# Optimization experiments

Hardware: AMD Instinct MI355X
Metric: run time of the kernel (lower is better)

The kernel has to match this reference:

```python
import jax, jax.numpy as jnp
import numpy as np

VOCAB, EMB, HID, LAYERS = 32000, 512, 512, 2
B, S = 16, 256


def setup_inputs() -> dict:
    key = jax.random.key(0)
    ks = jax.random.split(key, 8)
    x = jax.random.randint(ks[0], (B, S), 0, VOCAB)
    emb = jax.random.normal(ks[1], (VOCAB, EMB), dtype=jnp.float32) * 0.02
    # input_dim == hidden_dim == 512, so per-layer weights can be stacked
    Wih = jax.random.normal(ks[2], (LAYERS, 4 * HID, EMB), dtype=jnp.float32) * 0.05
    Whh = jax.random.normal(ks[3], (LAYERS, 4 * HID, HID), dtype=jnp.float32) * 0.05
    b = jax.random.normal(ks[4], (LAYERS, 4 * HID), dtype=jnp.float32) * 0.05
    fc_w = jax.random.normal(ks[5], (VOCAB, HID), dtype=jnp.float32) * 0.02
    fc_b = jnp.zeros((VOCAB,), dtype=jnp.float32)
    return {"x": x, "emb": emb, "Wih": Wih, "Whh": Whh, "b": b, "fc_w": fc_w, "fc_b": fc_b}


def reference(x, emb, Wih, Whh, b, fc_w, fc_b):
    L = Wih.shape[0]
    Bsz = x.shape[0]
    H = Whh.shape[-1]
    xe = emb[x]  # (B, S, E)
    h0 = jnp.zeros((L, Bsz, H), dtype=emb.dtype)
    c0 = jnp.zeros((L, Bsz, H), dtype=emb.dtype)

    def step(carry, xt):  # xt: (B, E)
        h, c = carry
        inp = xt
        hs, cs = [], []
        for l in range(L):  # small fixed layer loop
            gates = inp @ Wih[l].T + h[l] @ Whh[l].T + b[l]  # (B, 4H)
            i, f, g, o = jnp.split(gates, 4, axis=1)
            cn = jax.nn.sigmoid(f) * c[l] + jax.nn.sigmoid(i) * jnp.tanh(g)
            hn = jax.nn.sigmoid(o) * jnp.tanh(cn)
            hs.append(hn)
            cs.append(cn)
            inp = hn
        return (jnp.stack(hs), jnp.stack(cs)), inp

    _, outs = jax.lax.scan(step, (h0, c0), jnp.swapaxes(xe, 0, 1))  # outs: (S, B, H)
    outs = jnp.swapaxes(outs, 0, 1)  # (B, S, H); dropout is identity (eval)
    logits = outs @ fc_w.T + fc_b  # (B, S, V)
    return logits
```

## Files before the change

### kernel.cpp

```cpp
#include <hip/hip_runtime.h>
#include <hip/hip_bf16.h>

#define SEQ 256
#define NB 16
#define HID 512
#define VOC 32000

typedef short bf16x8 __attribute__((ext_vector_type(8)));
typedef float f32x4 __attribute__((ext_vector_type(4)));
typedef unsigned long long u64;

__device__ __forceinline__ void ld_lds16(const void* g, void* l) {
  __builtin_amdgcn_global_load_lds((const __attribute__((address_space(1))) void*)g,
                                   (__attribute__((address_space(3))) void*)l, 16, 0, 0);
}

__device__ __forceinline__ float sigf(float x) { return 1.0f / (1.0f + expf(-x)); }

__device__ __forceinline__ unsigned pk2(float a, float b) {
  __hip_bfloat16 ha = __float2bfloat16(a), hb = __float2bfloat16(b);
  unsigned short ua = *(unsigned short*)&ha, ub = *(unsigned short*)&hb;
  return (unsigned)ua | ((unsigned)ub << 16);
}

__device__ __forceinline__ u64 agload(const u64* p) {
  return __hip_atomic_load(p, __ATOMIC_RELAXED, __HIP_MEMORY_SCOPE_AGENT);
}
__device__ __forceinline__ void agstore(u64* p, u64 v) {
  __hip_atomic_store(p, v, __ATOMIC_RELAXED, __HIP_MEMORY_SCOPE_AGENT);
}

__device__ __forceinline__ void issue16(u64* q, const u64* base) {
#pragma unroll
  for (int s = 0; s < 4; ++s)
#pragma unroll
    for (int j = 0; j < 4; ++j) q[s * 4 + j] = agload(base + s * 256 + j * 16);
}
__device__ __forceinline__ void revalidate16(u64* q, const u64* base, unsigned tg) {
  for (;;) {
    int bad = 0;
#pragma unroll
    for (int i = 0; i < 16; ++i) bad |= ((unsigned)(q[i] >> 32) != tg);
    if (!__any(bad)) break;
    __builtin_amdgcn_s_sleep(1);
#pragma unroll
    for (int i = 0; i < 16; ++i)
      if ((unsigned)(q[i] >> 32) != tg)
        q[i] = agload(base + (i >> 2) * 256 + (i & 3) * 16);
  }
}

__device__ __forceinline__ void cvt8_hilo(const float* p, bf16x8* h8, bf16x8* l8) {
  union { unsigned short u[8]; bf16x8 v; } uh, ul;
#pragma unroll
  for (int i = 0; i < 8; ++i) {
    float v = p[i];
    __hip_bfloat16 h = __float2bfloat16(v);
    uh.u[i] = *(unsigned short*)&h;
    float rem = v - __bfloat162float(h);
    __hip_bfloat16 l = __float2bfloat16(rem);
    ul.u[i] = *(unsigned short*)&l;
  }
  *h8 = uh.v;
  *l8 = ul.v;
}

__global__ void embed_k(const int* __restrict__ x, const float* __restrict__ emb,
                        unsigned short* __restrict__ xe) {
  int bid = blockIdx.x;
  int t = bid >> 4, b = bid & 15;
  int tok = x[b * SEQ + t];
  const float4* src = (const float4*)(emb + (size_t)tok * HID);
  int e = threadIdx.x;
  float4 a = src[e * 2], c = src[e * 2 + 1];
  uint4 o;
  o.x = pk2(a.x, a.y); o.y = pk2(a.z, a.w);
  o.z = pk2(c.x, c.y); o.w = pk2(c.z, c.w);
  ((uint4*)(xe + (size_t)bid * HID))[e] = o;
}

__global__ void cvt_k(const float* __restrict__ in, uint4* __restrict__ out) {
  size_t i = (size_t)blockIdx.x * blockDim.x + threadIdx.x;
  const float4* in4 = (const float4*)in;
  float4 a = in4[i * 2], b = in4[i * 2 + 1];
  uint4 o;
  o.x = pk2(a.x, a.y); o.y = pk2(a.z, a.w);
  o.z = pk2(b.x, b.y); o.w = pk2(b.z, b.w);
  out[i] = o;
}

__global__ __launch_bounds__(256) void gx_gemm(const __hip_bfloat16* __restrict__ A,
                                               const __hip_bfloat16* __restrict__ Bw,
                                               unsigned short* __restrict__ C) {
  __shared__ __align__(16) unsigned short lds_a[128 * 32];
  __shared__ __align__(16) unsigned short lds_b[128 * 32];
  const int tid = threadIdx.x;
  const int lane = tid & 63, wid = tid >> 6;
  const int m0 = blockIdx.y * 128, n0 = blockIdx.x * 128;
  const char* Ab = (const char*)A;
  const char* Bb = (const char*)Bw;
  const int ra = tid >> 2, cb = (tid & 3) * 16;
  f32x4 acc[4][4] = {};
  const int wm = (wid >> 1) * 64, wn = (wid & 1) * 64;
  const int fr = lane & 15, fk = (lane >> 4) * 8;
  for (int k0 = 0; k0 < HID; k0 += 32) {
    ld_lds16(Ab + (size_t)(m0 + ra) * 1024 + k0 * 2 + cb, (char*)lds_a + wid * 1024);
    ld_lds16(Ab + (size_t)(m0 + 64 + ra) * 1024 + k0 * 2 + cb, (char*)lds_a + 4096 + wid * 1024);
    ld_lds16(Bb + (size_t)(n0 + ra) * 1024 + k0 * 2 + cb, (char*)lds_b + wid * 1024);
    ld_lds16(Bb + (size_t)(n0 + 64 + ra) * 1024 + k0 * 2 + cb, (char*)lds_b + 4096 + wid * 1024);
    __syncthreads();
    bf16x8 af[4], bf[4];
#pragma unroll
    for (int i = 0; i < 4; ++i) af[i] = *(const bf16x8*)&lds_a[(wm + i * 16 + fr) * 32 + fk];
#pragma unroll
    for (int j = 0; j < 4; ++j) bf[j] = *(const bf16x8*)&lds_b[(wn + j * 16 + fr) * 32 + fk];
#pragma unroll
    for (int i = 0; i < 4; ++i)
#pragma unroll
      for (int j = 0; j < 4; ++j)
        acc[i][j] = __builtin_amdgcn_mfma_f32_16x16x32_bf16(af[i], bf[j], acc[i][j], 0, 0, 0);
    __syncthreads();
  }
  const int cr = (lane >> 4) * 4, cc = lane & 15;
#pragma unroll
  for (int i = 0; i < 4; ++i)
#pragma unroll
    for (int jj = 0; jj < 4; ++jj) {
      size_t base = (size_t)(m0 + wm + i * 16 + cr) * 2048 + (n0 + wn + jj * 16 + cc);
#pragma unroll
      for (int r = 0; r < 4; ++r) {
        __hip_bfloat16 h = __float2bfloat16(acc[i][jj][r]);
        C[base + (size_t)r * 2048] = *(unsigned short*)&h;
      }
    }
}

__global__ __launch_bounds__(256) void lstm_k(
    const float* __restrict__ Wih, const float* __restrict__ Whh,
    const float* __restrict__ bias, const unsigned short* __restrict__ gxb,
    u64* __restrict__ h0r, u64* __restrict__ h1r, unsigned short* __restrict__ outs) {
  __shared__ float pbuf[4][16][17];
  const int tid = threadIdx.x, bid = blockIdx.x;
  const int lay = bid >> 7, r8 = bid & 127;
  const int hc0 = r8 * 4;
  const int wid = tid >> 6, lane = tid & 63;
  const int b16 = lane & 15, hi = lane >> 4;

  const int jrow = (b16 >> 2) * HID + hc0 + (b16 & 3);
  const int kb = wid * 128 + hi * 8;
  const float* wih_row = Wih + ((size_t)lay * 2048 + jrow) * HID;
  const float* whh_row = Whh + ((size_t)lay * 2048 + jrow) * HID;
  bf16x8 w0[4], w1[4], w2[4], w3[4];
#pragma unroll
  for (int s = 0; s < 4; ++s) {
    if (lay == 0) {
      cvt8_hilo(whh_row + kb + s * 32, &w0[s], &w1[s]);
      w2[s] = w0[s]; w3[s] = w1[s];
    } else {
      cvt8_hilo(wih_row + kb + s * 32, &w0[s], &w1[s]);
      cvt8_hilo(whh_row + kb + s * 32, &w2[s], &w3[s]);
    }
  }
  const int eb = lane & 15, ehl = lane >> 4;
  float bq[4];
#pragma unroll
  for (int q = 0; q < 4; ++q) bq[q] = bias[lay * 2048 + q * HID + hc0 + ehl];
  float c_reg = 0.f;
  const int lbase = wid * 1024 + hi * 64 + b16;

#pragma unroll 1
  for (int t = 0; t < SEQ; ++t) {
    f32x4 acc0 = {0.f, 0.f, 0.f, 0.f}, acc1 = {0.f, 0.f, 0.f, 0.f};
    float gxr[4] = {0.f, 0.f, 0.f, 0.f};
    if (lay == 0) {
      const u64* srcA = h0r + (size_t)t * 4096 + lbase;
      u64 qa[16];
      issue16(qa, srcA);
      if (wid == 0) {
        const unsigned short* gp = gxb + ((size_t)(t * 16 + eb)) * 2048 + hc0 + ehl;
#pragma unroll
        for (int q = 0; q < 4; ++q) {
          union { unsigned u; float f; } cv;
          cv.u = (unsigned)gp[q * HID] << 16;
          gxr[q] = cv.f;
        }
        asm volatile("" : "+v"(gxr[0]), "+v"(gxr[1]), "+v"(gxr[2]), "+v"(gxr[3]));
      }
      revalidate16(qa, srcA, (unsigned)t);
#pragma unroll
      for (int s = 0; s < 4; ++s) {
        union { unsigned u[4]; bf16x8 v; } bb;
#pragma unroll
        for (int j = 0; j < 4; ++j) bb.u[j] = (unsigned)qa[s * 4 + j];
        acc0 = __builtin_amdgcn_mfma_f32_16x16x32_bf16(w0[s], bb.v, acc0, 0, 0, 0);
        acc1 = __builtin_amdgcn_mfma_f32_16x16x32_bf16(w1[s], bb.v, acc1, 0, 0, 0);
      }
    } else {
      const u64* srcA = h0r + (size_t)(t + 1) * 4096 + lbase;
      const u64* srcB = h1r + (size_t)t * 4096 + lbase;
      u64 qb[16], qa[16];
      issue16(qb, srcB);
      issue16(qa, srcA);
      revalidate16(qb, srcB, (unsigned)t);
#pragma unroll
      for (int s = 0; s < 4; ++s) {
        union { unsigned u[4]; bf16x8 v; } bb;
#pragma unroll
        for (int j = 0; j < 4; ++j) bb.u[j] = (unsigned)qb[s * 4 + j];
        acc0 = __builtin_amdgcn_mfma_f32_16x16x32_bf16(w2[s], bb.v, acc0, 0, 0, 0);
        acc1 = __builtin_amdgcn_mfma_f32_16x16x32_bf16(w3[s], bb.v, acc1, 0, 0, 0);
      }
      revalidate16(qa, srcA, (unsigned)(t + 1));
#pragma unroll
      for (int s = 0; s < 4; ++s) {
        union { unsigned u[4]; bf16x8 v; } bb;
#pragma unroll
        for (int j = 0; j < 4; ++j) bb.u[j] = (unsigned)qa[s * 4 + j];
        acc0 = __builtin_amdgcn_mfma_f32_16x16x32_bf16(w0[s], bb.v, acc0, 0, 0, 0);
        acc1 = __builtin_amdgcn_mfma_f32_16x16x32_bf16(w1[s], bb.v, acc1, 0, 0, 0);
      }
    }
    f32x4 acc = acc0 + acc1;
#pragma unroll
    for (int rr = 0; rr < 4; ++rr) pbuf[wid][hi * 4 + rr][b16] = acc[rr];
    __syncthreads();

    if (wid == 0) {
      float pre[4];
#pragma unroll
      for (int q = 0; q < 4; ++q) {
        const int rl = q * 4 + ehl;
        pre[q] = bq[q] + gxr[q] + pbuf[0][rl][eb] + pbuf[1][rl][eb] +
                 pbuf[2][rl][eb] + pbuf[3][rl][eb];
      }
      float iv = sigf(pre[0]), fv = sigf(pre[1]);
      float gv = tanhf(pre[2]), ov = sigf(pre[3]);
      c_reg = fv * c_reg + iv * gv;
      float hn = ov * tanhf(c_reg);
      __hip_bfloat16 hh = __float2bfloat16(hn);
      int hb = (int)*(unsigned short*)&hh;
      int pr = __shfl_xor(hb, 16, 64);
      unsigned data32 = (unsigned)(unsigned short)hb | ((unsigned)(unsigned short)pr << 16);
      u64* ringo = (lay ? h1r : h0r) + (size_t)(t + 1) * 4096;
      if ((ehl & 1) == 0)
        agstore(ringo + (r8 * 2 + (ehl >> 1)) * 16 + eb,
                (u64)data32 | ((u64)(unsigned)(t + 1) << 32));
      if (lay) {
        unsigned d23 = (unsigned)__shfl((int)data32, eb + 32, 64);
        if (ehl == 0)
          *(u64*)(outs + ((size_t)(t * 16 + eb)) * 512 + hc0) = (u64)data32 | ((u64)d23 << 32);
      }
    }
    __syncthreads();
  }
}

__global__ __launch_bounds__(256) void fc_gemm(const __hip_bfloat16* __restrict__ A,
                                               const __hip_bfloat16* __restrict__ Bw,
                                               const float* __restrict__ bias,
                                               float* __restrict__ C) {
  __shared__ __align__(16) unsigned short lds_a[128 * 32];
  __shared__ __align__(16) unsigned short lds_b[128 * 32];
  const int tid = threadIdx.x;
  const int lane = tid & 63, wid = tid >> 6;
  const int m0 = blockIdx.y * 128, n0 = blockIdx.x * 128;
  const char* Ab = (const char*)A;
  const char* Bb = (const char*)Bw;
  const int ra = tid >> 2, cb = (tid & 3) * 16;
  f32x4 acc[4][4] = {};
  const int wm = (wid >> 1) * 64, wn = (wid & 1) * 64;
  const int fr = lane & 15, fk = (lane >> 4) * 8;
  for (int k0 = 0; k0 < HID; k0 += 32) {
    ld_lds16(Ab + (size_t)(m0 + ra) * 1024 + k0 * 2 + cb, (char*)lds_a + wid * 1024);
    ld_lds16(Ab + (size_t)(m0 + 64 + ra) * 1024 + k0 * 2 + cb, (char*)lds_a + 4096 + wid * 1024);
    ld_lds16(Bb + (size_t)(n0 + ra) * 1024 + k0 * 2 + cb, (char*)lds_b + wid * 1024);
    ld_lds16(Bb + (size_t)(n0 + 64 + ra) * 1024 + k0 * 2 + cb, (char*)lds_b + 4096 + wid * 1024);
    __syncthreads();
    bf16x8 af[4], bf[4];
#pragma unroll
    for (int i = 0; i < 4; ++i) af[i] = *(const bf16x8*)&lds_a[(wm + i * 16 + fr) * 32 + fk];
#pragma unroll
    for (int j = 0; j < 4; ++j) bf[j] = *(const bf16x8*)&lds_b[(wn + j * 16 + fr) * 32 + fk];
#pragma unroll
    for (int i = 0; i < 4; ++i)
#pragma unroll
      for (int j = 0; j < 4; ++j)
        acc[i][j] = __builtin_amdgcn_mfma_f32_16x16x32_bf16(af[i], bf[j], acc[i][j], 0, 0, 0);
    __syncthreads();
  }
  const int cr = (lane >> 4) * 4, cc = lane & 15;
  float bv[4];
#pragma unroll
  for (int jj = 0; jj < 4; ++jj) bv[jj] = bias[n0 + wn + jj * 16 + cc];
#pragma unroll
  for (int i = 0; i < 4; ++i) {
#pragma unroll
    for (int jj = 0; jj < 4; ++jj) {
#pragma unroll
      for (int rr = 0; rr < 4; ++rr) {
        int tok = m0 + wm + i * 16 + cr + rr;
        int orow = (tok & 15) * SEQ + (tok >> 4);
        C[(size_t)orow * VOC + (n0 + wn + jj * 16 + cc)] = acc[i][jj][rr] + bv[jj];
      }
    }
  }
}

extern "C" void kernel_launch(void* const* d_in, const int* in_sizes, int n_in,
                              void* d_out, int out_size, void* d_ws, size_t ws_size,
                              hipStream_t stream) {
  const int* x = (const int*)d_in[0];
  const float* emb = (const float*)d_in[1];
  const float* Wih = (const float*)d_in[2];
  const float* Whh = (const float*)d_in[3];
  const float* bias = (const float*)d_in[4];
  const float* fcw = (const float*)d_in[5];
  const float* fcb = (const float*)d_in[6];
  float* out = (float*)d_out;
  char* ws = (char*)d_ws;

  u64* h0r = (u64*)ws;
  u64* h1r = (u64*)(ws + 8421376);
  uint4* wih0_bf = (uint4*)(ws + 16842752);
  unsigned short* gxb = (unsigned short*)(ws + 18939904);
  unsigned short* xe = (unsigned short*)(ws + 35717120);
  unsigned short* outs = (unsigned short*)(ws + 35717120);
  uint4* fcw_bf = (uint4*)ws;

  hipMemsetAsync(ws, 0, 16842752, stream);
  embed_k<<<SEQ * NB, 64, 0, stream>>>(x, emb, xe);
  cvt_k<<<512, 256, 0, stream>>>(Wih, wih0_bf);
  gx_gemm<<<dim3(16, 32), 256, 0, stream>>>((const __hip_bfloat16*)xe,
                                            (const __hip_bfloat16*)wih0_bf, gxb);
  lstm_k<<<256, 256, 0, stream>>>(Wih, Whh, bias, gxb, h0r, h1r, outs);
  cvt_k<<<8000, 256, 0, stream>>>(fcw, fcw_bf);
  fc_gemm<<<dim3(250, 32), 256, 0, stream>>>((const __hip_bfloat16*)outs,
                                             (const __hip_bfloat16*)fcw_bf, fcb, out);
}
```

Measured before the change: 1.226 ms.

## Halve LSTM block count by giving each block eight hidden columns

The persistent LSTM kernel now runs 128 blocks instead of 256, with each block computing 8 hidden units (two 16-row MFMA tiles) per layer. Each block issues twice the MFMAs per step on the same loaded h vector, and the number of blocks polling the ring buffer and contending for synchronisation is halved. The revalidate spin now first polls a single element with a longer sleep before checking the rest, to cut memory polling traffic. The trade-off is more register pressure from the doubled weight fragments, a longer serial gate computation per block, and fewer CUs in use.

```diff
diff --git a/kernel.cpp b/kernel.cpp
--- a/kernel.cpp
+++ b/kernel.cpp
@@ -36,15 +36,22 @@
 #pragma unroll
     for (int j = 0; j < 4; ++j) q[s * 4 + j] = agload(base + s * 256 + j * 16);
 }
+
 __device__ __forceinline__ void revalidate16(u64* q, const u64* base, unsigned tg) {
   for (;;) {
+    bool ok = ((unsigned)(q[0] >> 32) == tg);
+    if (__all(ok)) break;
+    __builtin_amdgcn_s_sleep(2);
+    if (!ok) q[0] = agload(base);
+  }
+  for (;;) {
     int bad = 0;
 #pragma unroll
-    for (int i = 0; i < 16; ++i) bad |= ((unsigned)(q[i] >> 32) != tg);
+    for (int i = 1; i < 16; ++i) bad |= ((unsigned)(q[i] >> 32) != tg);
     if (!__any(bad)) break;
     __builtin_amdgcn_s_sleep(1);
 #pragma unroll
-    for (int i = 0; i < 16; ++i)
+    for (int i = 1; i < 16; ++i)
       if ((unsigned)(q[i] >> 32) != tg)
         q[i] = agload(base + (i >> 2) * 256 + (i & 3) * 16);
   }
@@ -135,43 +142,46 @@
     }
 }
 
-__global__ __launch_bounds__(256) void lstm_k(
+__global__ __launch_bounds__(256, 1) void lstm_k(
     const float* __restrict__ Wih, const float* __restrict__ Whh,
     const float* __restrict__ bias, const unsigned short* __restrict__ gxb,
     u64* __restrict__ h0r, u64* __restrict__ h1r, unsigned short* __restrict__ outs) {
-  __shared__ float pbuf[4][16][17];
+  __shared__ float pbuf[4][32][17];
   const int tid = threadIdx.x, bid = blockIdx.x;
-  const int lay = bid >> 7, r8 = bid & 127;
-  const int hc0 = r8 * 4;
+  const int lay = bid >> 6, r = bid & 63;
+  const int hc0 = r * 8;
   const int wid = tid >> 6, lane = tid & 63;
   const int b16 = lane & 15, hi = lane >> 4;
 
-  const int jrow = (b16 >> 2) * HID + hc0 + (b16 & 3);
   const int kb = wid * 128 + hi * 8;
-  const float* wih_row = Wih + ((size_t)lay * 2048 + jrow) * HID;
-  const float* whh_row = Whh + ((size_t)lay * 2048 + jrow) * HID;
-  bf16x8 w0[4], w1[4], w2[4], w3[4];
-#pragma unroll
-  for (int s = 0; s < 4; ++s) {
-    if (lay == 0) {
-      cvt8_hilo(whh_row + kb + s * 32, &w0[s], &w1[s]);
-      w2[s] = w0[s]; w3[s] = w1[s];
-    } else {
-      cvt8_hilo(wih_row + kb + s * 32, &w0[s], &w1[s]);
-      cvt8_hilo(whh_row + kb + s * 32, &w2[s], &w3[s]);
+  bf16x8 Wh[2][2][4], Wi[2][2][4];
+#pragma unroll
+  for (int m = 0; m < 2; ++m) {
+    const int jrow = (b16 >> 2) * HID + hc0 + m * 4 + (b16 & 3);
+    const float* whh_row = Whh + ((size_t)lay * 2048 + jrow) * HID;
+    const float* wih_row = Wih + ((size_t)lay * 2048 + jrow) * HID;
+#pragma unroll
+    for (int s = 0; s < 4; ++s) {
+      cvt8_hilo(whh_row + kb + s * 32, &Wh[m][0][s], &Wh[m][1][s]);
+      if (lay) cvt8_hilo(wih_row + kb + s * 32, &Wi[m][0][s], &Wi[m][1][s]);
+      else { Wi[m][0][s] = Wh[m][0][s]; Wi[m][1][s] = Wh[m][1][s]; }
     }
   }
   const int eb = lane & 15, ehl = lane >> 4;
-  float bq[4];
-#pragma unroll
-  for (int q = 0; q < 4; ++q) bq[q] = bias[lay * 2048 + q * HID + hc0 + ehl];
-  float c_reg = 0.f;
+  float bq[2][4];
+#pragma unroll
+  for (int m = 0; m < 2; ++m)
+#pragma unroll
+    for (int q = 0; q < 4; ++q)
+      bq[m][q] = bias[lay * 2048 + q * HID + hc0 + m * 4 + ehl];
+  float c0 = 0.f, c1 = 0.f;
   const int lbase = wid * 1024 + hi * 64 + b16;
 
 #pragma unroll 1
   for (int t = 0; t < SEQ; ++t) {
-    f32x4 acc0 = {0.f, 0.f, 0.f, 0.f}, acc1 = {0.f, 0.f, 0.f, 0.f};
-    float gxr[4] = {0.f, 0.f, 0.f, 0.f};
+    f32x4 ah0 = {0.f, 0.f, 0.f, 0.f}, al0 = {0.f, 0.f, 0.f, 0.f};
+    f32x4 ah1 = {0.f, 0.f, 0.f, 0.f}, al1 = {0.f, 0.f, 0.f, 0.f};
+    float gxr[2][4] = {};
     if (lay == 0) {
       const u64* srcA = h0r + (size_t)t * 4096 + lbase;
       u64 qa[16];
@@ -179,12 +189,14 @@
       if (wid == 0) {
         const unsigned short* gp = gxb + ((size_t)(t * 16 + eb)) * 2048 + hc0 + ehl;
 #pragma unroll
-        for (int q = 0; q < 4; ++q) {
-          union { unsigned u; float f; } cv;
-          cv.u = (unsigned)gp[q * HID] << 16;
-          gxr[q] = cv.f;
-        }
-        asm volatile("" : "+v"(gxr[0]), "+v"(gxr[1]), "+v"(gxr[2]), "+v"(gxr[3]));
+        for (int m = 0; m < 2; ++m)
+#pragma unroll
+          for (int q = 0; q < 4; ++q) {
+            union { unsigned u; float f; } cv;
+            cv.u = (unsigned)gp[m * 4 + q * HID] << 16;
+            gxr[m][q] = cv.f;
+            asm volatile("" : "+v"(gxr[m][q]));
+          }
       }
       revalidate16(qa, srcA, (unsigned)t);
 #pragma unroll
@@ -192,8 +204,10 @@
         union { unsigned u[4]; bf16x8 v; } bb;
 #pragma unroll
         for (int j = 0; j < 4; ++j) bb.u[j] = (unsigned)qa[s * 4 + j];
-        acc0 = __builtin_amdgcn_mfma_f32_16x16x32_bf16(w0[s], bb.v, acc0, 0, 0, 0);
-        acc1 = __builtin_amdgcn_mfma_f32_16x16x32_bf16(w1[s], bb.v, acc1, 0, 0, 0);
+        ah0 = __builtin_amdgcn_mfma_f32_16x16x32_bf16(Wh[0][0][s], bb.v, ah0, 0, 0, 0);
+        al0 = __builtin_amdgcn_mfma_f32_16x16x32_bf16(Wh[0][1][s], bb.v, al0, 0, 0, 0);
+        ah1 = __builtin_amdgcn_mfma_f32_16x16x32_bf16(Wh[1][0][s], bb.v, ah1, 0, 0, 0);
+        al1 = __builtin_amdgcn_mfma_f32_16x16x32_bf16(Wh[1][1][s], bb.v, al1, 0, 0, 0);
       }
     } else {
       const u64* srcA = h0r + (size_t)(t + 1) * 4096 + lbase;
@@ -207,8 +221,10 @@
         union { unsigned u[4]; bf16x8 v; } bb;
 #pragma unroll
         for (int j = 0; j < 4; ++j) bb.u[j] = (unsigned)qb[s * 4 + j];
-        acc0 = __builtin_amdgcn_mfma_f32_16x16x32_bf16(w2[s], bb.v, acc0, 0, 0, 0);
-        acc1 = __builtin_amdgcn_mfma_f32_16x16x32_bf16(w3[s], bb.v, acc1, 0, 0, 0);
+        ah0 = __builtin_amdgcn_mfma_f32_16x16x32_bf16(Wh[0][0][s], bb.v, ah0, 0, 0, 0);
+        al0 = __builtin_amdgcn_mfma_f32_16x16x32_bf16(Wh[0][1][s], bb.v, al0, 0, 0, 0);
+        ah1 = __builtin_amdgcn_mfma_f32_16x16x32_bf16(Wh[1][0][s], bb.v, ah1, 0, 0, 0);
+        al1 = __builtin_amdgcn_mfma_f32_16x16x32_bf16(Wh[1][1][s], bb.v, al1, 0, 0, 0);
       }
       revalidate16(qa, srcA, (unsigned)(t + 1));
 #pragma unroll
@@ -216,39 +232,53 @@
         union { unsigned u[4]; bf16x8 v; } bb;
 #pragma unroll
         for (int j = 0; j < 4; ++j) bb.u[j] = (unsigned)qa[s * 4 + j];
-        acc0 = __builtin_amdgcn_mfma_f32_16x16x32_bf16(w0[s], bb.v, acc0, 0, 0, 0);
-        acc1 = __builtin_amdgcn_mfma_f32_16x16x32_bf16(w1[s], bb.v, acc1, 0, 0, 0);
-      }
-    }
-    f32x4 acc = acc0 + acc1;
-#pragma unroll
-    for (int rr = 0; rr < 4; ++rr) pbuf[wid][hi * 4 + rr][b16] = acc[rr];
+        ah0 = __builtin_amdgcn_mfma_f32_16x16x32_bf16(Wi[0][0][s], bb.v, ah0, 0, 0, 0);
+        al0 = __builtin_amdgcn_mfma_f32_16x16x32_bf16(Wi[0][1][s], bb.v, al0, 0, 0, 0);
+        ah1 = __builtin_amdgcn_mfma_f32_16x16x32_bf16(Wi[1][0][s], bb.v, ah1, 0, 0, 0);
+        al1 = __builtin_amdgcn_mfma_f32_16x16x32_bf16(Wi[1][1][s], bb.v, al1, 0, 0, 0);
+      }
+    }
+    f32x4 am0 = ah0 + al0, am1 = ah1 + al1;
+#pragma unroll
+    for (int rr = 0; rr < 4; ++rr) {
+      pbuf[wid][hi * 4 + rr][b16] = am0[rr];
+      pbuf[wid][16 + hi * 4 + rr][b16] = am1[rr];
+    }
     __syncthreads();
 
     if (wid == 0) {
-      float pre[4];
-#pragma unroll
-      for (int q = 0; q < 4; ++q) {
-        const int rl = q * 4 + ehl;
-        pre[q] = bq[q] + gxr[q] + pbuf[0][rl][eb] + pbuf[1][rl][eb] +
-                 pbuf[2][rl][eb] + pbuf[3][rl][eb];
-      }
-      float iv = sigf(pre[0]), fv = sigf(pre[1]);
-      float gv = tanhf(pre[2]), ov = sigf(pre[3]);
-      c_reg = fv * c_reg + iv * gv;
-      float hn = ov * tanhf(c_reg);
-      __hip_bfloat16 hh = __float2bfloat16(hn);
-      int hb = (int)*(unsigned short*)&hh;
-      int pr = __shfl_xor(hb, 16, 64);
-      unsigned data32 = (unsigned)(unsigned short)hb | ((unsigned)(unsigned short)pr << 16);
+      float hn[2];
+#pragma unroll
+      for (int m = 0; m < 2; ++m) {
+        float pre[4];
+#pragma unroll
+        for (int q = 0; q < 4; ++q) {
+          const int rl = m * 16 + q * 4 + ehl;
+          pre[q] = bq[m][q] + gxr[m][q] + pbuf[0][rl][eb] + pbuf[1][rl][eb] +
+                   pbuf[2][rl][eb] + pbuf[3][rl][eb];
+        }
+        float iv = sigf(pre[0]), fv = sigf(pre[1]);
+        float gv = tanhf(pre[2]), ov = sigf(pre[3]);
+        float& cm = m ? c1 : c0;
+        cm = fv * cm + iv * gv;
+        hn[m] = ov * tanhf(cm);
+      }
+      __hip_bfloat16 h0b = __float2bfloat16(hn[0]), h1b = __float2bfloat16(hn[1]);
+      int hb0 = (int)*(unsigned short*)&h0b, hb1 = (int)*(unsigned short*)&h1b;
+      int pr0 = __shfl_xor(hb0, 16, 64), pr1 = __shfl_xor(hb1, 16, 64);
+      unsigned d0 = (unsigned)(unsigned short)hb0 | ((unsigned)(unsigned short)pr0 << 16);
+      unsigned d1 = (unsigned)(unsigned short)hb1 | ((unsigned)(unsigned short)pr1 << 16);
+      unsigned d0o = (unsigned)__shfl((int)d0, eb + 32, 64);
+      unsigned d1o = (unsigned)__shfl((int)d1, eb + 32, 64);
+      u64 tagw = (u64)(unsigned)(t + 1) << 32;
       u64* ringo = (lay ? h1r : h0r) + (size_t)(t + 1) * 4096;
-      if ((ehl & 1) == 0)
-        agstore(ringo + (r8 * 2 + (ehl >> 1)) * 16 + eb,
-                (u64)data32 | ((u64)(unsigned)(t + 1) << 32));
-      if (lay) {
-        unsigned d23 = (unsigned)__shfl((int)data32, eb + 32, 64);
-        if (ehl == 0)
-          *(u64*)(outs + ((size_t)(t * 16 + eb)) * 512 + hc0) = (u64)data32 | ((u64)d23 << 32);
+      if ((ehl & 1) == 0) {
+        agstore(ringo + ((r * 4 + (ehl >> 1)) * 16 + eb), (u64)d0 | tagw);
+        agstore(ringo + ((r * 4 + 2 + (ehl >> 1)) * 16 + eb), (u64)d1 | tagw);
+      }
+      if (lay && ehl == 0) {
+        uint4 ov4 = {d0, d0o, d1, d1o};
+        *(uint4*)(outs + ((size_t)(t * 16 + eb)) * 512 + hc0) = ov4;
       }
     }
     __syncthreads();
@@ -332,7 +362,7 @@
   cvt_k<<<512, 256, 0, stream>>>(Wih, wih0_bf);
   gx_gemm<<<dim3(16, 32), 256, 0, stream>>>((const __hip_bfloat16*)xe,
                                             (const __hip_bfloat16*)wih0_bf, gxb);
-  lstm_k<<<256, 256, 0, stream>>>(Wih, Whh, bias, gxb, h0r, h1r, outs);
+  lstm_k<<<128, 256, 0, stream>>>(Wih, Whh, bias, gxb, h0r, h1r, outs);
   cvt_k<<<8000, 256, 0, stream>>>(fcw, fcw_bf);
   fc_gemm<<<dim3(250, 32), 256, 0, stream>>>((const __hip_bfloat16*)outs,
                                              (const __hip_bfloat16*)fcw_bf, fcb, out);
```

Result: slower. 1.449 ms (+18.1%).

## Repartition persistent LSTM kernel to 64 workgroups of 512 threads, 16 hidden units each

Applied to the files above, without the earlier changes.

The recurrent kernel is restructured so each active workgroup owns 16 hidden columns with 8 waves. It launches 256 blocks but keeps only blocks where (bid&7)<2, which presumably spreads active workgroups across XCDs/CUs. Layer 1 splits the input-hidden and hidden-hidden halves across wave groups instead of running them serially in each wave. The intent is to cut the number of workgroups exchanging h through the global ring, so each step has fewer cross-CU dependencies and less polling overhead. In exchange each workgroup carries more weight registers and does more MFMA work per step, with a larger LDS reduction.

```diff
diff --git a/kernel.cpp b/kernel.cpp
--- a/kernel.cpp
+++ b/kernel.cpp
@@ -30,23 +30,22 @@
   __hip_atomic_store(p, v, __ATOMIC_RELAXED, __HIP_MEMORY_SCOPE_AGENT);
 }
 
-__device__ __forceinline__ void issue16(u64* q, const u64* base) {
-#pragma unroll
-  for (int s = 0; s < 4; ++s)
-#pragma unroll
-    for (int j = 0; j < 4; ++j) q[s * 4 + j] = agload(base + s * 256 + j * 16);
-}
-__device__ __forceinline__ void revalidate16(u64* q, const u64* base, unsigned tg) {
+template <int N>
+__device__ __forceinline__ void issueN(u64* q, const u64* base) {
+#pragma unroll
+  for (int i = 0; i < N; ++i) q[i] = agload(base + (i >> 2) * 256 + (i & 3) * 16);
+}
+template <int N>
+__device__ __forceinline__ void revalN(u64* q, const u64* base, unsigned tg) {
   for (;;) {
     int bad = 0;
 #pragma unroll
-    for (int i = 0; i < 16; ++i) bad |= ((unsigned)(q[i] >> 32) != tg);
+    for (int i = 0; i < N; ++i) bad |= ((unsigned)(q[i] >> 32) != tg);
     if (!__any(bad)) break;
     __builtin_amdgcn_s_sleep(1);
 #pragma unroll
-    for (int i = 0; i < 16; ++i)
-      if ((unsigned)(q[i] >> 32) != tg)
-        q[i] = agload(base + (i >> 2) * 256 + (i & 3) * 16);
+    for (int i = 0; i < N; ++i)
+      if ((unsigned)(q[i] >> 32) != tg) q[i] = agload(base + (i >> 2) * 256 + (i & 3) * 16);
   }
 }
 
@@ -135,103 +134,117 @@
     }
 }
 
-__global__ __launch_bounds__(256) void lstm_k(
+__global__ __launch_bounds__(512, 1) void lstm_k(
     const float* __restrict__ Wih, const float* __restrict__ Whh,
     const float* __restrict__ bias, const unsigned short* __restrict__ gxb,
     u64* __restrict__ h0r, u64* __restrict__ h1r, unsigned short* __restrict__ outs) {
-  __shared__ float pbuf[4][16][17];
-  const int tid = threadIdx.x, bid = blockIdx.x;
-  const int lay = bid >> 7, r8 = bid & 127;
-  const int hc0 = r8 * 4;
-  const int wid = tid >> 6, lane = tid & 63;
+  const int bid = blockIdx.x;
+  const int sel = bid & 7;
+  if (sel > 1) return;
+  const int lay = sel, r = bid >> 3;
+  const int hc0 = r * 16;
+  const int tid = threadIdx.x;
+  const int wv = tid >> 6, lane = tid & 63;
   const int b16 = lane & 15, hi = lane >> 4;
-
-  const int jrow = (b16 >> 2) * HID + hc0 + (b16 & 3);
-  const int kb = wid * 128 + hi * 8;
-  const float* wih_row = Wih + ((size_t)lay * 2048 + jrow) * HID;
-  const float* whh_row = Whh + ((size_t)lay * 2048 + jrow) * HID;
-  bf16x8 w0[4], w1[4], w2[4], w3[4];
-#pragma unroll
-  for (int s = 0; s < 4; ++s) {
+  __shared__ float pbuf[8][64][17];
+
+  bf16x8 W[4][2][4];
+  {
+    const int q = b16 >> 2, c = b16 & 3;
     if (lay == 0) {
-      cvt8_hilo(whh_row + kb + s * 32, &w0[s], &w1[s]);
-      w2[s] = w0[s]; w3[s] = w1[s];
+#pragma unroll
+      for (int m = 0; m < 4; ++m) {
+        const float* row = Whh + (size_t)(q * HID + hc0 + m * 4 + c) * HID;
+#pragma unroll
+        for (int s = 0; s < 2; ++s)
+          cvt8_hilo(row + wv * 64 + s * 32 + hi * 8, &W[m][0][s], &W[m][1][s]);
+      }
     } else {
-      cvt8_hilo(wih_row + kb + s * 32, &w0[s], &w1[s]);
-      cvt8_hilo(whh_row + kb + s * 32, &w2[s], &w3[s]);
-    }
-  }
-  const int eb = lane & 15, ehl = lane >> 4;
+      const float* basep = (wv < 4) ? Wih : Whh;
+      const int kb = (wv & 3) * 128;
+#pragma unroll
+      for (int m = 0; m < 4; ++m) {
+        const float* row = basep + (size_t)(2048 + q * HID + hc0 + m * 4 + c) * HID;
+#pragma unroll
+        for (int s = 0; s < 4; ++s)
+          cvt8_hilo(row + kb + s * 32 + hi * 8, &W[m][0][s], &W[m][1][s]);
+      }
+    }
+  }
+  const int eb = b16, ehl = hi;
+  const bool epi = (wv < 4);
   float bq[4];
-#pragma unroll
-  for (int q = 0; q < 4; ++q) bq[q] = bias[lay * 2048 + q * HID + hc0 + ehl];
+  if (epi) {
+#pragma unroll
+    for (int q = 0; q < 4; ++q) bq[q] = bias[lay * 2048 + q * HID + hc0 + wv * 4 + ehl];
+  }
   float c_reg = 0.f;
-  const int lbase = wid * 1024 + hi * 64 + b16;
 
 #pragma unroll 1
   for (int t = 0; t < SEQ; ++t) {
-    f32x4 acc0 = {0.f, 0.f, 0.f, 0.f}, acc1 = {0.f, 0.f, 0.f, 0.f};
+    f32x4 acc[4] = {{0.f, 0.f, 0.f, 0.f}, {0.f, 0.f, 0.f, 0.f},
+                    {0.f, 0.f, 0.f, 0.f}, {0.f, 0.f, 0.f, 0.f}};
     float gxr[4] = {0.f, 0.f, 0.f, 0.f};
     if (lay == 0) {
-      const u64* srcA = h0r + (size_t)t * 4096 + lbase;
-      u64 qa[16];
-      issue16(qa, srcA);
-      if (wid == 0) {
-        const unsigned short* gp = gxb + ((size_t)(t * 16 + eb)) * 2048 + hc0 + ehl;
+      const u64* src = h0r + (size_t)t * 4096 + (wv * 512 + hi * 64 + b16);
+      u64 q8[8];
+      issueN<8>(q8, src);
+      if (epi) {
+        const unsigned short* gp = gxb + ((size_t)(t * 16 + eb)) * 2048 + hc0 + wv * 4 + ehl;
 #pragma unroll
         for (int q = 0; q < 4; ++q) {
           union { unsigned u; float f; } cv;
           cv.u = (unsigned)gp[q * HID] << 16;
           gxr[q] = cv.f;
+          asm volatile("" : "+v"(gxr[q]));
         }
-        asm volatile("" : "+v"(gxr[0]), "+v"(gxr[1]), "+v"(gxr[2]), "+v"(gxr[3]));
-      }
-      revalidate16(qa, srcA, (unsigned)t);
+      }
+      revalN<8>(q8, src, (unsigned)t);
+#pragma unroll
+      for (int s = 0; s < 2; ++s) {
+        union { unsigned u[4]; bf16x8 v; } bb;
+#pragma unroll
+        for (int j = 0; j < 4; ++j) bb.u[j] = (unsigned)q8[s * 4 + j];
+#pragma unroll
+        for (int m = 0; m < 4; ++m) {
+          acc[m] = __builtin_amdgcn_mfma_f32_16x16x32_bf16(W[m][0][s], bb.v, acc[m], 0, 0, 0);
+          acc[m] = __builtin_amdgcn_mfma_f32_16x16x32_bf16(W[m][1][s], bb.v, acc[m], 0, 0, 0);
+        }
+      }
+    } else {
+      const u64* src = ((wv < 4) ? (h0r + (size_t)(t + 1) * 4096)
+                                 : (h1r + (size_t)t * 4096))
+                       + ((wv & 3) * 1024 + hi * 64 + b16);
+      const unsigned tg = (wv < 4) ? (unsigned)(t + 1) : (unsigned)t;
+      u64 q16[16];
+      issueN<16>(q16, src);
+      revalN<16>(q16, src, tg);
 #pragma unroll
       for (int s = 0; s < 4; ++s) {
         union { unsigned u[4]; bf16x8 v; } bb;
 #pragma unroll
-        for (int j = 0; j < 4; ++j) bb.u[j] = (unsigned)qa[s * 4 + j];
-        acc0 = __builtin_amdgcn_mfma_f32_16x16x32_bf16(w0[s], bb.v, acc0, 0, 0, 0);
-        acc1 = __builtin_amdgcn_mfma_f32_16x16x32_bf16(w1[s], bb.v, acc1, 0, 0, 0);
-      }
-    } else {
-      const u64* srcA = h0r + (size_t)(t + 1) * 4096 + lbase;
-      const u64* srcB = h1r + (size_t)t * 4096 + lbase;
-      u64 qb[16], qa[16];
-      issue16(qb, srcB);
-      issue16(qa, srcA);
-      revalidate16(qb, srcB, (unsigned)t);
-#pragma unroll
-      for (int s = 0; s < 4; ++s) {
-        union { unsigned u[4]; bf16x8 v; } bb;
-#pragma unroll
-        for (int j = 0; j < 4; ++j) bb.u[j] = (unsigned)qb[s * 4 + j];
-        acc0 = __builtin_amdgcn_mfma_f32_16x16x32_bf16(w2[s], bb.v, acc0, 0, 0, 0);
-        acc1 = __builtin_amdgcn_mfma_f32_16x16x32_bf16(w3[s], bb.v, acc1, 0, 0, 0);
-      }
-      revalidate16(qa, srcA, (unsigned)(t + 1));
-#pragma unroll
-      for (int s = 0; s < 4; ++s) {
-        union { unsigned u[4]; bf16x8 v; } bb;
-#pragma unroll
-        for (int j = 0; j < 4; ++j) bb.u[j] = (unsigned)qa[s * 4 + j];
-        acc0 = __builtin_amdgcn_mfma_f32_16x16x32_bf16(w0[s], bb.v, acc0, 0, 0, 0);
-        acc1 = __builtin_amdgcn_mfma_f32_16x16x32_bf16(w1[s], bb.v, acc1, 0, 0, 0);
-      }
-    }
-    f32x4 acc = acc0 + acc1;
-#pragma unroll
-    for (int rr = 0; rr < 4; ++rr) pbuf[wid][hi * 4 + rr][b16] = acc[rr];
-    __syncthreads();
-
-    if (wid == 0) {
+        for (int j = 0; j < 4; ++j) bb.u[j] = (unsigned)q16[s * 4 + j];
+#pragma unroll
+        for (int m = 0; m < 4; ++m) {
+          acc[m] = __builtin_amdgcn_mfma_f32_16x16x32_bf16(W[m][0][s], bb.v, acc[m], 0, 0, 0);
+          acc[m] = __builtin_amdgcn_mfma_f32_16x16x32_bf16(W[m][1][s], bb.v, acc[m], 0, 0, 0);
+        }
+      }
+    }
+#pragma unroll
+    for (int m = 0; m < 4; ++m)
+#pragma unroll
+      for (int rr = 0; rr < 4; ++rr) pbuf[wv][m * 16 + hi * 4 + rr][b16] = acc[m][rr];
+    __syncthreads();
+
+    if (epi) {
       float pre[4];
 #pragma unroll
       for (int q = 0; q < 4; ++q) {
-        const int rl = q * 4 + ehl;
-        pre[q] = bq[q] + gxr[q] + pbuf[0][rl][eb] + pbuf[1][rl][eb] +
-                 pbuf[2][rl][eb] + pbuf[3][rl][eb];
+        const int rl = wv * 16 + q * 4 + ehl;
+        float s0 = pbuf[0][rl][eb] + pbuf[1][rl][eb] + pbuf[2][rl][eb] + pbuf[3][rl][eb];
+        float s1 = pbuf[4][rl][eb] + pbuf[5][rl][eb] + pbuf[6][rl][eb] + pbuf[7][rl][eb];
+        pre[q] = bq[q] + gxr[q] + s0 + s1;
       }
       float iv = sigf(pre[0]), fv = sigf(pre[1]);
       float gv = tanhf(pre[2]), ov = sigf(pre[3]);
@@ -241,14 +254,17 @@
       int hb = (int)*(unsigned short*)&hh;
       int pr = __shfl_xor(hb, 16, 64);
       unsigned data32 = (unsigned)(unsigned short)hb | ((unsigned)(unsigned short)pr << 16);
+      u64 tagw = (u64)(unsigned)(t + 1) << 32;
       u64* ringo = (lay ? h1r : h0r) + (size_t)(t + 1) * 4096;
-      if ((ehl & 1) == 0)
-        agstore(ringo + (r8 * 2 + (ehl >> 1)) * 16 + eb,
-                (u64)data32 | ((u64)(unsigned)(t + 1) << 32));
+      if ((ehl & 1) == 0) {
+        const int cp = r * 8 + wv * 2 + (ehl >> 1);
+        agstore(ringo + cp * 16 + eb, (u64)data32 | tagw);
+      }
       if (lay) {
-        unsigned d23 = (unsigned)__shfl((int)data32, eb + 32, 64);
+        unsigned d2 = (unsigned)__shfl((int)data32, eb + 32, 64);
         if (ehl == 0)
-          *(u64*)(outs + ((size_t)(t * 16 + eb)) * 512 + hc0) = (u64)data32 | ((u64)d23 << 32);
+          *(u64*)(outs + ((size_t)(t * 16 + eb)) * 512 + hc0 + wv * 4) =
+              (u64)data32 | ((u64)d2 << 32);
       }
     }
     __syncthreads();
@@ -332,7 +348,7 @@
   cvt_k<<<512, 256, 0, stream>>>(Wih, wih0_bf);
   gx_gemm<<<dim3(16, 32), 256, 0, stream>>>((const __hip_bfloat16*)xe,
                                             (const __hip_bfloat16*)wih0_bf, gxb);
-  lstm_k<<<256, 256, 0, stream>>>(Wih, Whh, bias, gxb, h0r, h1r, outs);
+  lstm_k<<<256, 512, 0, stream>>>(Wih, Whh, bias, gxb, h0r, h1r, outs);
   cvt_k<<<8000, 256, 0, stream>>>(fcw, fcw_bf);
   fc_gemm<<<dim3(250, 32), 256, 0, stream>>>((const __hip_bfloat16*)outs,
                                              (const __hip_bfloat16*)fcw_bf, fcb, out);
```

After: 1.282 ms. +4.6%, slower.
